# Performance work log

Measured on AMD Instinct MI355X. Metric: run time of the kernel, lower is better.

The kernel has to match this reference:

```python
import jax, jax.numpy as jnp
import numpy as np

BETA = 0.2
EPS = 1e-10
N_LAYERS = 5  # same shared-weight gconv applied 5 times


def setup_inputs() -> dict:
    key = jax.random.key(0)
    ks = jax.random.split(key, 5)
    B, J, C = 16384, 17, 128
    x = jax.random.normal(ks[0], (B, J, C), dtype=jnp.float32)
    x0 = jax.random.normal(ks[1], (B, J, C), dtype=jnp.float32)
    adj = jax.random.uniform(ks[2], (J, J), dtype=jnp.float32)
    adj = 0.5 * (adj + adj.T)  # symmetric skeleton-like adjacency
    W0 = jax.random.normal(ks[3], (C, C), dtype=jnp.float32) * (1.0 / np.sqrt(C))
    W1 = jax.random.normal(ks[4], (C, C), dtype=jnp.float32) * (1.0 / np.sqrt(C))
    b = jnp.zeros((C,), dtype=jnp.float32)
    gamma = jnp.ones((C,), dtype=jnp.float32)
    beta_ln = jnp.zeros((C,), dtype=jnp.float32)
    return {"x": x, "x0": x0, "adj": adj, "W0": W0, "W1": W1, "b": b,
            "gamma": gamma, "beta_ln": beta_ln}


def _gconv(x, x0, adj_diag, adj_off, W0, W1, b):
    # self-loop term uses W0, neighbor aggregation uses W1
    h0 = jnp.einsum('bjc,cd->bjd', x, W0)
    h1 = jnp.einsum('bjc,cd->bjd', x, W1)
    out = adj_diag[None, :, None] * h0 + jnp.einsum('jk,bkd->bjd', adj_off, h1)
    return BETA * x0 + (1.0 - BETA) * out + b


def _layernorm(x, gamma, beta_ln):
    mu = jnp.mean(x, axis=-1, keepdims=True)
    var = jnp.mean(jnp.square(x - mu), axis=-1, keepdims=True)
    return (x - mu) * jax.lax.rsqrt(var + EPS) * gamma + beta_ln


def reference(x, x0, adj, W0, W1, b, gamma, beta_ln):
    J = adj.shape[0]
    eye = jnp.eye(J, dtype=adj.dtype)
    adj_diag = jnp.diagonal(adj)          # [J] self-loop weights
    adj_off = adj * (1.0 - eye)           # [J,J] neighbor weights
    for _ in range(N_LAYERS):
        x = _gconv(x, x0, adj_diag, adj_off, W0, W1, b)
    return _layernorm(x, gamma, beta_ln)
```

## Files before the change

kernel.cpp:

```cpp
#include <hip/hip_runtime.h>
#include <stdint.h>

typedef unsigned short u16;
typedef unsigned int   u32;
typedef _Float16 f16x4 __attribute__((ext_vector_type(4)));
typedef _Float16 f16x8 __attribute__((ext_vector_type(8)));
typedef __attribute__((ext_vector_type(16))) float f16v;

#define JJ 17
#define CC 128
#define BB 7
#define ROWS (BB*JJ)
#define PP 128
#define XP 132
#define HT 136
#define NLAYERS 5
#define NT 1024

#define XH_OFF   0
#define HT_OFF   (PP*XP*2)
#define W_OFF    (HT_OFF + PP*HT*2)
#define LDS_BYTES (W_OFF + 2*PP*XP*2)

#define MFMA __builtin_amdgcn_mfma_f32_32x32x16_f16

__device__ __forceinline__ u16 h2b(_Float16 h) {
  union { _Float16 h; u16 b; } c; c.h = h; return c.b;
}
__device__ __forceinline__ _Float16 b2h(u16 b) {
  union { u16 b; _Float16 h; } c; c.b = b; return c.h;
}
__device__ __forceinline__ f16x8 cmbh(f16x4 a, f16x4 b) {
  f16x8 r;
  r[0]=a[0]; r[1]=a[1]; r[2]=a[2]; r[3]=a[3];
  r[4]=b[0]; r[5]=b[1]; r[6]=b[2]; r[7]=b[3];
  return r;
}
__device__ __forceinline__ float wred(float v) {
  #pragma unroll
  for (int m = 32; m >= 1; m >>= 1) v += __shfl_xor(v, m, 64);
  return v;
}
__device__ __forceinline__ f16x8 u4f8(uint4 v) {
  union { uint4 u; f16x8 f; } c; c.u = v; return c.f;
}

__global__ void __launch_bounds__(256)
wprep(const float* __restrict__ W0, const float* __restrict__ W1,
      const float* __restrict__ adj, u16* __restrict__ wsH,
      u16* __restrict__ amixf)
{
  __shared__ float wt[64*130];
  const int w01 = blockIdx.x;
  const float* Wp = w01 ? W1 : W0;
  const int tid = threadIdx.x;
  if (w01 == 0) {
    for (int t = tid; t < 8192; t += 256) {
      int e  = t & 7, nl = (t >> 3) & 31, g = (t >> 8) & 1;
      int i  = (t >> 9) & 3, wm = t >> 11;
      const int kslo = (wm==0)?0:(wm==1)?1:(wm==2)?3:4;
      int row = wm*32 + nl;
      int k   = (kslo + i)*16 + 8*g + e;
      float v = 0.f;
      if (row < ROWS && k < ROWS && (row/JJ) == (k/JJ) && (row%JJ) != (k%JJ))
        v = 0.8f * adj[(row%JJ)*JJ + (k%JJ)];
      amixf[t] = h2b((_Float16)v);
    }
  }
  for (int kh = 0; kh < 2; ++kh) {
    if (kh) __syncthreads();
    #pragma unroll
    for (int i = 0; i < 32; ++i) {
      int idx = tid + i*256;
      int kk = idx >> 7, col = idx & 127;
      wt[kk*130 + col] = Wp[(kh*64 + kk)*128 + col];
    }
    __syncthreads();
    #pragma unroll
    for (int i = 0; i < 32; ++i) {
      int idx = tid + i*256;
      int col = idx >> 6, kk = idx & 63;
      wsH[(size_t)(w01*128 + col)*128 + kh*64 + kk] = h2b((_Float16)wt[kk*130 + col]);
    }
  }
}

__global__ void __launch_bounds__(NT, 4)
gconv_fused(const float* __restrict__ x, const float* __restrict__ x0,
            const float* __restrict__ adj, const u16* __restrict__ wsH,
            const u16* __restrict__ amixf, const float* __restrict__ bvec,
            const float* __restrict__ gamma, const float* __restrict__ beta,
            float* __restrict__ out, int totRows)
{
  extern __shared__ char smem[];
  u16* xh   = (u16*)(smem + XH_OFF);
  u16* h1t  = (u16*)(smem + HT_OFF);
  u16* wlds = (u16*)(smem + W_OFF);

  const int tid  = threadIdx.x;
  const int lane = tid & 63;
  const int wid  = tid >> 6;
  const int wm   = wid >> 2;
  const int wn   = wid & 3;
  const int g    = lane >> 5;
  const int nl   = lane & 31;
  const int ccol = wn*32 + nl;
  const int grow0 = blockIdx.x * ROWS;
  const int kslo = (wm==0)?0:(wm==1)?1:(wm==2)?3:4;

  f16x8 amx[4];
  #pragma unroll
  for (int i = 0; i < 4; ++i)
    amx[i] = u4f8(*(const uint4*)&amixf[(((wm*4+i)*2)+g)*256 + nl*8]);

  {
    int el = tid * 32;
    int w01 = el >> 14, rem = el & 16383;
    int col = rem >> 7, k0 = rem & 127;
    const u16* src = wsH + el;
    u16* dst = &wlds[(w01*128 + col)*XP + k0];
    #pragma unroll
    for (int c = 0; c < 8; ++c)
      *(uint2*)(dst + c*4) = *(const uint2*)(src + c*4);
  }

  u32 x0p[8], dpk[8];
  #pragma unroll
  for (int qp = 0; qp < 8; ++qp) {
    u32 pk = 0, dk = 0;
    #pragma unroll
    for (int h = 0; h < 2; ++h) {
      int q = qp*2 + h;
      int row = wm*32 + (q&3) + 8*(q>>2) + 4*g;
      int grow = grow0 + row;
      u16 xb = 0, db = 0;
      if (row < ROWS && grow < totRows) {
        xb = h2b((_Float16)x0[(size_t)grow*CC + ccol]);
        int j = row % JJ;
        db = h2b((_Float16)(0.8f * adj[j*JJ + j]));
      }
      pk |= ((u32)xb) << (16*h);
      dk |= ((u32)db) << (16*h);
    }
    x0p[qp] = pk; dpk[qp] = dk;
  }
  const float bias_c = bvec[ccol];

  #pragma unroll
  for (int i = 0; i < 4; ++i) {
    int el4 = tid + i*NT;
    int r = el4 >> 5, c4 = (el4 & 31) << 2;
    float4 v = make_float4(0.f, 0.f, 0.f, 0.f);
    if (r < ROWS && (grow0 + r) < totRows)
      v = *(const float4*)&x[(size_t)(grow0 + r)*CC + c4];
    u16 s0 = h2b((_Float16)v.x), s1 = h2b((_Float16)v.y);
    u16 s2 = h2b((_Float16)v.z), s3 = h2b((_Float16)v.w);
    *(uint2*)&xh[r*XP + c4] = make_uint2((u32)s0 | ((u32)s1<<16), (u32)s2 | ((u32)s3<<16));
  }
  __syncthreads();

  const int arow = (wm*32 + nl)*XP;
  const int bb0  = ccol*XP;
  const int bb1  = bb0 + 128*XP;
  const int htb  = ccol*HT + 8*g;

  #pragma unroll 1
  for (int layer = 0; layer < NLAYERS; ++layer) {
    f16v acc0, acc1;
    #pragma unroll
    for (int i = 0; i < 16; ++i) { acc0[i] = 0.f; acc1[i] = 0.f; }

    #pragma unroll
    for (int ks = 0; ks < 8; ++ks) {
      const int o = ks*16 + 8*g;
      f16x8 ah = cmbh(*(const f16x4*)&xh[arow + o],   *(const f16x4*)&xh[arow + o + 4]);
      f16x8 b0 = cmbh(*(const f16x4*)&wlds[bb0 + o],  *(const f16x4*)&wlds[bb0 + o + 4]);
      f16x8 b1 = cmbh(*(const f16x4*)&wlds[bb1 + o],  *(const f16x4*)&wlds[bb1 + o + 4]);
      acc0 = MFMA(ah, b0, acc0, 0, 0, 0);
      acc1 = MFMA(ah, b1, acc1, 0, 0, 0);
      __builtin_amdgcn_sched_barrier(0);
    }

    #pragma unroll
    for (int qp = 0; qp < 8; ++qp) {
      int q = qp*2;
      int row = wm*32 + (q&3) + 8*(q>>2) + 4*g;
      u32 pk = (u32)h2b((_Float16)acc1[q]) | ((u32)h2b((_Float16)acc1[q+1]) << 16);
      *(u32*)&h1t[ccol*HT + row] = pk;
    }
    __syncthreads();

    #pragma unroll
    for (int i = 0; i < 16; ++i) acc1[i] = 0.f;
    #pragma unroll
    for (int i = 0; i < 4; ++i) {
      f16x8 hb = u4f8(*(const uint4*)&h1t[htb + (kslo + i)*16]);
      acc1 = MFMA(amx[i], hb, acc1, 0, 0, 0);
    }

    #pragma unroll
    for (int q = 0; q < 16; ++q) {
      int row = wm*32 + (q&3) + 8*(q>>2) + 4*g;
      float x0v = (float)b2h((u16)(x0p[q>>1] >> (16*(q&1))));
      float dg  = (float)b2h((u16)(dpk[q>>1] >> (16*(q&1))));
      float v = 0.2f*x0v + dg*acc0[q] + acc1[q] + bias_c;
      xh[row*XP + ccol] = h2b((_Float16)v);
    }
    __syncthreads();
  }

  float ga = gamma[lane], g2 = gamma[64+lane];
  float ba = beta[lane],  b2f = beta[64+lane];
  #pragma unroll 1
  for (int i = 0; i < 8; ++i) {
    int r = wid + 16*i;
    if (r >= ROWS) continue;
    int grow = grow0 + r;
    if (grow >= totRows) continue;
    float xa = (float)b2h(xh[r*XP + lane]);
    float xc = (float)b2h(xh[r*XP + 64 + lane]);
    float mu = wred(xa + xc) * (1.f/128.f);
    float da = xa - mu, dc = xc - mu;
    float vs = wred(da*da + dc*dc) * (1.f/128.f);
    float rs = rsqrtf(vs + 1e-10f);
    size_t ob = (size_t)grow*CC;
    out[ob + lane]      = da*rs*ga + ba;
    out[ob + 64 + lane] = dc*rs*g2 + b2f;
  }
}

extern "C" void kernel_launch(void* const* d_in, const int* in_sizes, int n_in,
                              void* d_out, int out_size, void* d_ws, size_t ws_size,
                              hipStream_t stream) {
  const float* x   = (const float*)d_in[0];
  const float* x0  = (const float*)d_in[1];
  const float* adj = (const float*)d_in[2];
  const float* W0  = (const float*)d_in[3];
  const float* W1  = (const float*)d_in[4];
  const float* bv  = (const float*)d_in[5];
  const float* ga  = (const float*)d_in[6];
  const float* be  = (const float*)d_in[7];
  u16* wsH   = (u16*)d_ws;
  u16* amixf = (u16*)((char*)d_ws + 65536);
  int totRows = in_sizes[0] / CC;
  int nBatch  = totRows / JJ;
  int grid    = (nBatch + BB - 1) / BB;
  wprep<<<dim3(2), dim3(256), 0, stream>>>(W0, W1, adj, wsH, amixf);
  hipFuncSetAttribute((const void*)gconv_fused,
                      hipFuncAttributeMaxDynamicSharedMemorySize, LDS_BYTES);
  gconv_fused<<<dim3(grid), dim3(NT), LDS_BYTES, stream>>>(
      x, x0, adj, wsH, amixf, bv, ga, be, (float*)d_out, totRows);
}
```

Measured before the change: 418.3 us.

## Halve block size, stream weights from global, alias LDS buffers to raise occupancy

The block shrinks from 1024 to 512 threads, and each wave now computes two 32-row M tiles. The W0/W1 fragments are read directly from global or L2 with a one-step register prefetch instead of being staged in LDS. The x and h1-transpose buffers share one LDS region, protected by extra barriers, and the diagonal weights move to a small LDS table, cutting LDS to about 36KB so more blocks fit per CU. The trade-off is repeated global weight loads every layer, more barriers per layer, and higher register pressure from doubled accumulators.

```diff
diff --git a/kernel.cpp b/kernel.cpp
--- a/kernel.cpp
+++ b/kernel.cpp
@@ -3,7 +3,6 @@
 
 typedef unsigned short u16;
 typedef unsigned int   u32;
-typedef _Float16 f16x4 __attribute__((ext_vector_type(4)));
 typedef _Float16 f16x8 __attribute__((ext_vector_type(8)));
 typedef __attribute__((ext_vector_type(16))) float f16v;
 
@@ -13,14 +12,12 @@
 #define ROWS (BB*JJ)
 #define PP 128
 #define XP 132
-#define HT 136
+#define HTP 140
 #define NLAYERS 5
-#define NT 1024
-
-#define XH_OFF   0
-#define HT_OFF   (PP*XP*2)
-#define W_OFF    (HT_OFF + PP*HT*2)
-#define LDS_BYTES (W_OFF + 2*PP*XP*2)
+#define NT 512
+
+#define DIAG_OFF 35840
+#define LDS_BYTES (DIAG_OFF + 512)
 
 #define MFMA __builtin_amdgcn_mfma_f32_32x32x16_f16
 
@@ -29,12 +26,6 @@
 }
 __device__ __forceinline__ _Float16 b2h(u16 b) {
   union { u16 b; _Float16 h; } c; c.b = b; return c.h;
-}
-__device__ __forceinline__ f16x8 cmbh(f16x4 a, f16x4 b) {
-  f16x8 r;
-  r[0]=a[0]; r[1]=a[1]; r[2]=a[2]; r[3]=a[3];
-  r[4]=b[0]; r[5]=b[1]; r[6]=b[2]; r[7]=b[3];
-  return r;
 }
 __device__ __forceinline__ float wred(float v) {
   #pragma unroll
@@ -43,6 +34,11 @@
 }
 __device__ __forceinline__ f16x8 u4f8(uint4 v) {
   union { uint4 u; f16x8 f; } c; c.u = v; return c.f;
+}
+__device__ __forceinline__ f16x8 mk8(uint2 a, uint2 b) {
+  union { uint4 u; f16x8 f; } c;
+  c.u.x = a.x; c.u.y = a.y; c.u.z = b.x; c.u.w = b.y;
+  return c.f;
 }
 
 __global__ void __launch_bounds__(256)
@@ -57,9 +53,9 @@
   if (w01 == 0) {
     for (int t = tid; t < 8192; t += 256) {
       int e  = t & 7, nl = (t >> 3) & 31, g = (t >> 8) & 1;
-      int i  = (t >> 9) & 3, wm = t >> 11;
-      const int kslo = (wm==0)?0:(wm==1)?1:(wm==2)?3:4;
-      int row = wm*32 + nl;
+      int i  = (t >> 9) & 3, tt = t >> 11;
+      const int kslo = (tt==0)?0:(tt==1)?1:(tt==2)?3:4;
+      int row = tt*32 + nl;
       int k   = (kslo + i)*16 + 8*g + e;
       float v = 0.f;
       if (row < ROWS && k < ROWS && (row/JJ) == (k/JJ) && (row%JJ) != (k%JJ))
@@ -93,9 +89,9 @@
             float* __restrict__ out, int totRows)
 {
   extern __shared__ char smem[];
-  u16* xh   = (u16*)(smem + XH_OFF);
-  u16* h1t  = (u16*)(smem + HT_OFF);
-  u16* wlds = (u16*)(smem + W_OFF);
+  u16*   xh    = (u16*)smem;
+  u16*   h1t   = (u16*)smem;
+  float* diag8 = (float*)(smem + DIAG_OFF);
 
   const int tid  = threadIdx.x;
   const int lane = tid & 63;
@@ -106,48 +102,29 @@
   const int nl   = lane & 31;
   const int ccol = wn*32 + nl;
   const int grow0 = blockIdx.x * ROWS;
-  const int kslo = (wm==0)?0:(wm==1)?1:(wm==2)?3:4;
-
-  f16x8 amx[4];
+
+  u32 x0p[2][8];
   #pragma unroll
-  for (int i = 0; i < 4; ++i)
-    amx[i] = u4f8(*(const uint4*)&amixf[(((wm*4+i)*2)+g)*256 + nl*8]);
-
-  {
-    int el = tid * 32;
-    int w01 = el >> 14, rem = el & 16383;
-    int col = rem >> 7, k0 = rem & 127;
-    const u16* src = wsH + el;
-    u16* dst = &wlds[(w01*128 + col)*XP + k0];
-    #pragma unroll
-    for (int c = 0; c < 8; ++c)
-      *(uint2*)(dst + c*4) = *(const uint2*)(src + c*4);
-  }
-
-  u32 x0p[8], dpk[8];
+  for (int mt = 0; mt < 2; ++mt)
+    #pragma unroll
+    for (int qp = 0; qp < 8; ++qp) {
+      u32 pk = 0;
+      #pragma unroll
+      for (int h = 0; h < 2; ++h) {
+        int q = qp*2 + h;
+        int row = wm*64 + mt*32 + (q&3) + 8*(q>>2) + 4*g;
+        int grow = grow0 + row;
+        u16 bits = 0;
+        if (row < ROWS && grow < totRows)
+          bits = h2b((_Float16)(0.2f * x0[(size_t)grow*CC + ccol]));
+        pk |= ((u32)bits) << (16*h);
+      }
+      x0p[mt][qp] = pk;
+    }
+  const float bias_c = bvec[ccol];
+
   #pragma unroll
-  for (int qp = 0; qp < 8; ++qp) {
-    u32 pk = 0, dk = 0;
-    #pragma unroll
-    for (int h = 0; h < 2; ++h) {
-      int q = qp*2 + h;
-      int row = wm*32 + (q&3) + 8*(q>>2) + 4*g;
-      int grow = grow0 + row;
-      u16 xb = 0, db = 0;
-      if (row < ROWS && grow < totRows) {
-        xb = h2b((_Float16)x0[(size_t)grow*CC + ccol]);
-        int j = row % JJ;
-        db = h2b((_Float16)(0.8f * adj[j*JJ + j]));
-      }
-      pk |= ((u32)xb) << (16*h);
-      dk |= ((u32)db) << (16*h);
-    }
-    x0p[qp] = pk; dpk[qp] = dk;
-  }
-  const float bias_c = bvec[ccol];
-
-  #pragma unroll
-  for (int i = 0; i < 4; ++i) {
+  for (int i = 0; i < 8; ++i) {
     int el4 = tid + i*NT;
     int r = el4 >> 5, c4 = (el4 & 31) << 2;
     float4 v = make_float4(0.f, 0.f, 0.f, 0.f);
@@ -157,63 +134,91 @@
     u16 s2 = h2b((_Float16)v.z), s3 = h2b((_Float16)v.w);
     *(uint2*)&xh[r*XP + c4] = make_uint2((u32)s0 | ((u32)s1<<16), (u32)s2 | ((u32)s3<<16));
   }
+  if (tid < PP) {
+    int j = tid % JJ;
+    diag8[tid] = (tid < ROWS) ? 0.8f * adj[j*JJ + j] : 0.f;
+  }
   __syncthreads();
 
-  const int arow = (wm*32 + nl)*XP;
-  const int bb0  = ccol*XP;
-  const int bb1  = bb0 + 128*XP;
-  const int htb  = ccol*HT + 8*g;
+  const u16* w0p = wsH + (size_t)ccol*128 + 8*g;
+  const u16* w1p = wsH + (size_t)(128 + ccol)*128 + 8*g;
 
   #pragma unroll 1
   for (int layer = 0; layer < NLAYERS; ++layer) {
-    f16v acc0, acc1;
-    #pragma unroll
-    for (int i = 0; i < 16; ++i) { acc0[i] = 0.f; acc1[i] = 0.f; }
-
+    f16v acc0[2], acc1[2];
+    #pragma unroll
+    for (int mt = 0; mt < 2; ++mt)
+      #pragma unroll
+      for (int i = 0; i < 16; ++i) { acc0[mt][i] = 0.f; acc1[mt][i] = 0.f; }
+
+    f16x8 b0 = u4f8(*(const uint4*)(w0p));
+    f16x8 b1 = u4f8(*(const uint4*)(w1p));
     #pragma unroll
     for (int ks = 0; ks < 8; ++ks) {
-      const int o = ks*16 + 8*g;
-      f16x8 ah = cmbh(*(const f16x4*)&xh[arow + o],   *(const f16x4*)&xh[arow + o + 4]);
-      f16x8 b0 = cmbh(*(const f16x4*)&wlds[bb0 + o],  *(const f16x4*)&wlds[bb0 + o + 4]);
-      f16x8 b1 = cmbh(*(const f16x4*)&wlds[bb1 + o],  *(const f16x4*)&wlds[bb1 + o + 4]);
-      acc0 = MFMA(ah, b0, acc0, 0, 0, 0);
-      acc1 = MFMA(ah, b1, acc1, 0, 0, 0);
+      f16x8 nb0 = b0, nb1 = b1;
+      if (ks < 7) {
+        nb0 = u4f8(*(const uint4*)(w0p + (ks+1)*16));
+        nb1 = u4f8(*(const uint4*)(w1p + (ks+1)*16));
+      }
+      #pragma unroll
+      for (int mt = 0; mt < 2; ++mt) {
+        const int xb = (wm*64 + mt*32 + nl)*XP + ks*16 + 8*g;
+        f16x8 ah = mk8(*(const uint2*)&xh[xb], *(const uint2*)&xh[xb+4]);
+        acc0[mt] = MFMA(ah, b0, acc0[mt], 0, 0, 0);
+        acc1[mt] = MFMA(ah, b1, acc1[mt], 0, 0, 0);
+      }
       __builtin_amdgcn_sched_barrier(0);
-    }
-
-    #pragma unroll
-    for (int qp = 0; qp < 8; ++qp) {
-      int q = qp*2;
-      int row = wm*32 + (q&3) + 8*(q>>2) + 4*g;
-      u32 pk = (u32)h2b((_Float16)acc1[q]) | ((u32)h2b((_Float16)acc1[q+1]) << 16);
-      *(u32*)&h1t[ccol*HT + row] = pk;
-    }
-    __syncthreads();
-
-    #pragma unroll
-    for (int i = 0; i < 16; ++i) acc1[i] = 0.f;
-    #pragma unroll
-    for (int i = 0; i < 4; ++i) {
-      f16x8 hb = u4f8(*(const uint4*)&h1t[htb + (kslo + i)*16]);
-      acc1 = MFMA(amx[i], hb, acc1, 0, 0, 0);
-    }
-
-    #pragma unroll
-    for (int q = 0; q < 16; ++q) {
-      int row = wm*32 + (q&3) + 8*(q>>2) + 4*g;
-      float x0v = (float)b2h((u16)(x0p[q>>1] >> (16*(q&1))));
-      float dg  = (float)b2h((u16)(dpk[q>>1] >> (16*(q&1))));
-      float v = 0.2f*x0v + dg*acc0[q] + acc1[q] + bias_c;
-      xh[row*XP + ccol] = h2b((_Float16)v);
-    }
+      b0 = nb0; b1 = nb1;
+    }
+    __syncthreads();
+
+    #pragma unroll
+    for (int mt = 0; mt < 2; ++mt)
+      #pragma unroll
+      for (int qp = 0; qp < 8; ++qp) {
+        int q = qp*2;
+        int row = wm*64 + mt*32 + (q&3) + 8*(q>>2) + 4*g;
+        u32 pk = (u32)h2b((_Float16)acc1[mt][q]) | ((u32)h2b((_Float16)acc1[mt][q+1]) << 16);
+        *(u32*)&h1t[ccol*HTP + row] = pk;
+      }
+    __syncthreads();
+
+    #pragma unroll
+    for (int mt = 0; mt < 2; ++mt) {
+      const int t = wm*2 + mt;
+      const int kslo = (t==0)?0:(t==1)?1:(t==2)?3:4;
+      f16x8 am[4];
+      #pragma unroll
+      for (int i = 0; i < 4; ++i)
+        am[i] = u4f8(*(const uint4*)&amixf[(((t*4+i)*2)+g)*256 + nl*8]);
+      #pragma unroll
+      for (int i = 0; i < 16; ++i) acc1[mt][i] = 0.f;
+      #pragma unroll
+      for (int i = 0; i < 4; ++i) {
+        const int hidx = ccol*HTP + (kslo + i)*16 + 8*g;
+        f16x8 hb = mk8(*(const uint2*)&h1t[hidx], *(const uint2*)&h1t[hidx+4]);
+        acc1[mt] = MFMA(am[i], hb, acc1[mt], 0, 0, 0);
+      }
+    }
+    __syncthreads();
+
+    #pragma unroll
+    for (int mt = 0; mt < 2; ++mt)
+      #pragma unroll
+      for (int q = 0; q < 16; ++q) {
+        int row = wm*64 + mt*32 + (q&3) + 8*(q>>2) + 4*g;
+        float x0v = (float)b2h((u16)(x0p[mt][q>>1] >> (16*(q&1))));
+        float v = x0v + diag8[row]*acc0[mt][q] + acc1[mt][q] + bias_c;
+        xh[row*XP + ccol] = h2b((_Float16)v);
+      }
     __syncthreads();
   }
 
   float ga = gamma[lane], g2 = gamma[64+lane];
   float ba = beta[lane],  b2f = beta[64+lane];
   #pragma unroll 1
-  for (int i = 0; i < 8; ++i) {
-    int r = wid + 16*i;
+  for (int i = 0; i < 16; ++i) {
+    int r = wid + 8*i;
     if (r >= ROWS) continue;
     int grow = grow0 + r;
     if (grow >= totRows) continue;
@@ -246,8 +251,6 @@
   int nBatch  = totRows / JJ;
   int grid    = (nBatch + BB - 1) / BB;
   wprep<<<dim3(2), dim3(256), 0, stream>>>(W0, W1, adj, wsH, amixf);
-  hipFuncSetAttribute((const void*)gconv_fused,
-                      hipFuncAttributeMaxDynamicSharedMemorySize, LDS_BYTES);
   gconv_fused<<<dim3(grid), dim3(NT), LDS_BYTES, stream>>>(
       x, x0, adj, wsH, amixf, bv, ga, be, (float*)d_out, totRows);
 }
```

Measured after the change: 563.4 us. +34.7%, slower.
